# Kernel tuning notes

Hardware: AMD Instinct MI355X
Metric: run time of the kernel (lower is better)

## Reference

```python
import jax, jax.numpy as jnp
import numpy as np

D_MODEL = 512
NHEAD = 8
HEAD_DIM = D_MODEL // NHEAD
DFF = 2048
RANK = 64
L = 1024
N = 8
EPS = 1e-5


def _layer_norm(x, g, b):
    m = jnp.mean(x, axis=-1, keepdims=True)
    v = jnp.mean(jnp.square(x - m), axis=-1, keepdims=True)
    return (x - m) * jax.lax.rsqrt(v + EPS) * g + b


def setup_inputs() -> dict:
    key = jax.random.key(0)
    ks = jax.random.split(key, 20)
    s = 1.0 / np.sqrt(D_MODEL)
    inp = {
        "q": jax.random.normal(ks[0], (L, N, D_MODEL), jnp.float32),
        "k": jax.random.normal(ks[1], (L, N, D_MODEL), jnp.float32),
        "v": jax.random.normal(ks[2], (L, N, D_MODEL), jnp.float32),
        # attention projections, stored (in, out) so x @ W
        "Wq": jax.random.normal(ks[3], (D_MODEL, D_MODEL), jnp.float32) * s,
        "bq": jnp.zeros((D_MODEL,), jnp.float32),
        "Wk": jax.random.normal(ks[4], (D_MODEL, D_MODEL), jnp.float32) * s,
        "bk": jnp.zeros((D_MODEL,), jnp.float32),
        "Wv": jax.random.normal(ks[5], (D_MODEL, D_MODEL), jnp.float32) * s,
        "bv": jnp.zeros((D_MODEL,), jnp.float32),
        "Wo": jax.random.normal(ks[6], (D_MODEL, D_MODEL), jnp.float32) * s,
        "bo": jnp.zeros((D_MODEL,), jnp.float32),
        "topk": jnp.float32(0.3),  # learned scalar, k = int(S * sigmoid(topk))
        "A1": jax.random.normal(ks[7], (D_MODEL, RANK), jnp.float32) * s,
        "B1": jax.random.normal(ks[8], (RANK, DFF), jnp.float32) / np.sqrt(RANK),
        "A2": jax.random.normal(ks[9], (DFF, RANK), jnp.float32) / np.sqrt(DFF),
        "B2": jax.random.normal(ks[10], (RANK, D_MODEL), jnp.float32) / np.sqrt(RANK),
        "g1": jnp.ones((D_MODEL,), jnp.float32),
        "be1": jnp.zeros((D_MODEL,), jnp.float32),
        "g2": jnp.ones((D_MODEL,), jnp.float32),
        "be2": jnp.zeros((D_MODEL,), jnp.float32),
    }
    return inp


def reference(q, k, v, Wq, bq, Wk, bk, Wv, bv, Wo, bo, topk,
              A1, B1, A2, B2, g1, be1, g2, be2):
    Lq, Nb, E = q.shape
    S = k.shape[0]
    H, Dh = NHEAD, HEAD_DIM

    # projections -> (N, L, H, Dh)
    qh = (q @ Wq + bq).reshape(Lq, Nb, H, Dh).transpose(1, 0, 2, 3)
    kh = (k @ Wk + bk).reshape(S, Nb, H, Dh).transpose(1, 0, 2, 3)
    vh = (v @ Wv + bv).reshape(S, Nb, H, Dh).transpose(1, 0, 2, 3)

    scores = jnp.einsum('nlhd,nshd->nlhs', qh, kh) / jnp.sqrt(jnp.float32(Dh))

    # dynamic top-k mask: keep the k = int(S * sigmoid(topk)) largest per row
    k_keep = (S * jax.nn.sigmoid(topk)).astype(jnp.int32)  # 588 for topk=0.3
    sorted_desc = jnp.sort(scores, axis=-1)[..., ::-1]
    idx = jnp.broadcast_to(k_keep - 1, scores.shape[:-1])[..., None]
    thresh = jnp.take_along_axis(sorted_desc, idx, axis=-1)  # k-th largest
    masked = jnp.where(scores >= thresh, scores, -jnp.inf)
    attn_w = jax.nn.softmax(masked, axis=-1)

    # note original flattens (d, h) order: 'nlhs,nshd->nldh' then view(L,N,E)
    ao = jnp.einsum('nlhs,nshd->nldh', attn_w, vh)
    ao = ao.transpose(1, 0, 2, 3).reshape(Lq, Nb, E)
    attn_out = ao @ Wo + bo

    src = _layer_norm(q + attn_out, g1, be1)
    ffn = jax.nn.relu(src @ A1 @ B1) @ A2 @ B2
    src = _layer_norm(src + ffn, g2, be2)
    return src
```

## Files before the change

kernel.cpp:

```cpp
#include <hip/hip_runtime.h>

typedef unsigned short u16;
typedef unsigned int u32;
using s16x8 = __attribute__((ext_vector_type(8))) short;
using s16x4 = __attribute__((ext_vector_type(4))) short;
using u16x4 = __attribute__((ext_vector_type(4))) unsigned short;
using u32x4 = __attribute__((ext_vector_type(4))) unsigned int;
using f32x4 = __attribute__((ext_vector_type(4))) float;

__device__ __forceinline__ u16 f2bf(float f) {
  unsigned int u = __float_as_uint(f);
  u += 0x7FFFu + ((u >> 16) & 1u);
  return (u16)(u >> 16);
}
__device__ __forceinline__ float bf2f(u16 b) {
  return __uint_as_float(((u32)b) << 16);
}
__device__ __forceinline__ u32 pkbf(float a, float b) {
  u32 r;
  asm("v_cvt_pk_bf16_f32 %0, %1, %2" : "=v"(r) : "v"(a), "v"(b));
  return r;
}
__device__ __forceinline__ u32 f2key(float f) {
  u32 u = __float_as_uint(f);
  u32 flip = (u32)((int)u >> 31) | 0x80000000u;
  return (u ^ flip) >> 16;
}
__device__ __forceinline__ float key2f(u32 k) {
  u32 t = k << 16;
  u32 msk = ((int)t < 0) ? 0x80000000u : 0xFFFF0000u;
  return __uint_as_float(t ^ msk);
}

__global__ __launch_bounds__(256) void prep_all(
    const float* __restrict__ q, const float* __restrict__ k, const float* __restrict__ v,
    const float* __restrict__ Wq, const float* __restrict__ Wk, const float* __restrict__ Wv,
    const float* __restrict__ Wo, const float* __restrict__ A1, const float* __restrict__ B1,
    const float* __restrict__ A2, const float* __restrict__ B2,
    u16* __restrict__ qb, u16* __restrict__ kb, u16* __restrict__ vb,
    u16* __restrict__ WqT, u16* __restrict__ WkT, u16* __restrict__ WvT, u16* __restrict__ WoT,
    u16* __restrict__ A1T, u16* __restrict__ B1T, u16* __restrict__ A2T, u16* __restrict__ B2T) {
  __shared__ u16 t[64][68];
  int b = blockIdx.x, tid = threadIdx.x;
  if (b < 12288) {
    const float* src = b < 4096 ? q : (b < 8192 ? k : v);
    u16* dst = b < 4096 ? qb : (b < 8192 ? kb : vb);
    int i = (b & 4095) * 256 + tid;
    float4 f = ((const float4*)src)[i];
    u16x4 o;
    o[0] = f2bf(f.x); o[1] = f2bf(f.y); o[2] = f2bf(f.z); o[3] = f2bf(f.w);
    ((u16x4*)dst)[i] = o;
    return;
  }
  b -= 12288;
  const float* src; u16* dst; int base, R, C;
  if (b < 64)        { src = Wq; dst = WqT; base = 0;   R = 512;  C = 512; }
  else if (b < 128)  { src = Wk; dst = WkT; base = 64;  R = 512;  C = 512; }
  else if (b < 192)  { src = Wv; dst = WvT; base = 128; R = 512;  C = 512; }
  else if (b < 256)  { src = Wo; dst = WoT; base = 192; R = 512;  C = 512; }
  else if (b < 264)  { src = A1; dst = A1T; base = 256; R = 512;  C = 64;  }
  else if (b < 296)  { src = B1; dst = B1T; base = 264; R = 64;   C = 2048;}
  else if (b < 328)  { src = A2; dst = A2T; base = 296; R = 2048; C = 64;  }
  else               { src = B2; dst = B2T; base = 328; R = 64;   C = 512; }
  int ti = b - base;
  int tpr = C >> 6;
  int r0 = (ti / tpr) * 64, c0 = (ti % tpr) * 64;
#pragma unroll
  for (int i = 0; i < 4; ++i) {
    int r = i * 16 + (tid >> 4), c = (tid & 15) * 4;
    float4 f = *(const float4*)&src[(size_t)(r0 + r) * C + c0 + c];
    t[r][c] = f2bf(f.x); t[r][c + 1] = f2bf(f.y);
    t[r][c + 2] = f2bf(f.z); t[r][c + 3] = f2bf(f.w);
  }
  __syncthreads();
#pragma unroll
  for (int i = 0; i < 4; ++i) {
    int cc = i * 16 + (tid >> 4), rr = (tid & 15) * 4;
    u16x4 o;
    o[0] = t[rr][cc]; o[1] = t[rr + 1][cc]; o[2] = t[rr + 2][cc]; o[3] = t[rr + 3][cc];
    *(u16x4*)&dst[(size_t)(c0 + cc) * R + r0 + rr] = o;
  }
}

__global__ __launch_bounds__(256, 4) void qkv_fused(
    const u16* __restrict__ qb, const u16* __restrict__ kb, const u16* __restrict__ vb,
    const u16* __restrict__ WqT, const u16* __restrict__ WkT, const u16* __restrict__ WvT,
    const float* __restrict__ bq, const float* __restrict__ bk, const float* __restrict__ bv,
    u16* __restrict__ Qw, u16* __restrict__ Kw, u16* __restrict__ Vw) {
  __shared__ __align__(16) u16 As[128][72];
  __shared__ __align__(16) u16 Bs[128][72];
  const int z = blockIdx.z;
  const u16* A = z == 0 ? qb : (z == 1 ? kb : vb);
  const u16* Bt = z == 0 ? WqT : (z == 1 ? WkT : WvT);
  const float* bias = z == 0 ? bq : (z == 1 ? bk : bv);
  u16* outp = z == 0 ? Qw : (z == 1 ? Kw : Vw);

  const int tid = threadIdx.x;
  const int m0 = blockIdx.y * 128, n0 = blockIdx.x * 128;
  const int lane = tid & 63, wid = tid >> 6;
  const int l16 = lane & 15, hi = lane >> 4;
  const int wr = (wid >> 1) * 64, wc = (wid & 1) * 64;

  f32x4 acc[4][4];
#pragma unroll
  for (int i = 0; i < 4; ++i)
#pragma unroll
    for (int j = 0; j < 4; ++j) acc[i][j] = (f32x4){0.f, 0.f, 0.f, 0.f};

  for (int k0 = 0; k0 < 512; k0 += 64) {
    if (k0) __syncthreads();
#pragma unroll
    for (int i = 0; i < 4; ++i) {
      int idx = i * 256 + tid;
      int r = idx >> 3, cc = (idx & 7) * 8;
      *(s16x8*)&As[r][cc] = *(const s16x8*)&A[(size_t)(m0 + r) * 512 + k0 + cc];
      *(s16x8*)&Bs[r][cc] = *(const s16x8*)&Bt[(size_t)(n0 + r) * 512 + k0 + cc];
    }
    __syncthreads();
#pragma unroll
    for (int kk = 0; kk < 2; ++kk) {
      const int kb_ = kk * 32 + hi * 8;
      s16x8 af[4], bf[4];
#pragma unroll
      for (int mf = 0; mf < 4; ++mf) af[mf] = *(const s16x8*)&As[wr + mf * 16 + l16][kb_];
#pragma unroll
      for (int nf = 0; nf < 4; ++nf) bf[nf] = *(const s16x8*)&Bs[wc + nf * 16 + l16][kb_];
#pragma unroll
      for (int mf = 0; mf < 4; ++mf)
#pragma unroll
        for (int nf = 0; nf < 4; ++nf)
          acc[mf][nf] = __builtin_amdgcn_mfma_f32_16x16x32_bf16(af[mf], bf[nf], acc[mf][nf], 0, 0, 0);
    }
  }

#pragma unroll
  for (int mf = 0; mf < 4; ++mf)
#pragma unroll
    for (int nf = 0; nf < 4; ++nf)
#pragma unroll
      for (int i = 0; i < 4; ++i) {
        int row = m0 + wr + mf * 16 + hi * 4 + i;
        int col = n0 + wc + nf * 16 + l16;
        float val = acc[mf][nf][i] + bias[col];
        if (z == 0) val *= 0.18033688f;
        int l = row >> 3, n = row & 7, hh = col >> 6, d = col & 63;
        if (z < 2)
          outp[(((size_t)(n * 8 + hh) * 1024 + l) << 6) + d] = f2bf(val);
        else
          outp[((size_t)(n * 8 + hh) * 64 + d) * 1024 + l] = f2bf(val);
      }
}

__global__ __launch_bounds__(512, 4) void attn_kernel(const u16* __restrict__ Qw,
                                                      const u16* __restrict__ Kw,
                                                      const u16* __restrict__ Vw,
                                                      const float* __restrict__ topk,
                                                      u16* __restrict__ ao) {
  __shared__ __align__(16) u16 scb[32 * 1024];
  __shared__ __align__(16) u16 Qt[32][72];
  __shared__ float invs[32];
  const int tid = threadIdx.x, lane = tid & 63, wid = tid >> 6;
  const int l16 = lane & 15, hi = lane >> 4;
  const int mb = blockIdx.x, nh = blockIdx.y;

  const int kkeep = (int)(1024.f / (1.f + __expf(-topk[0])));

  {
    int r = tid >> 4, dc = (tid & 15) << 2;
    *(s16x4*)&Qt[r][dc] =
        *(const s16x4*)&Qw[((size_t)nh * 1024 + mb * 32 + r) * 64 + dc];
  }
  __syncthreads();

  {
    const u16* Kb = Kw + (size_t)nh * 1024 * 64;
    s16x8 bq0[2], bq1[2];
#pragma unroll
    for (int qh = 0; qh < 2; ++qh) {
      bq0[qh] = *(const s16x8*)&Qt[qh * 16 + l16][hi * 8];
      bq1[qh] = *(const s16x8*)&Qt[qh * 16 + l16][32 + hi * 8];
    }
    const int s0 = wid * 128;
    const size_t kbase = (size_t)(s0 + l16) * 64 + hi * 8;
    s16x8 c0 = *(const s16x8*)&Kb[kbase];
    s16x8 c1 = *(const s16x8*)&Kb[kbase + 32];
#pragma unroll
    for (int nf = 0; nf < 8; ++nf) {
      s16x8 n0_, n1_;
      if (nf < 7) {
        const size_t nb = kbase + (size_t)(nf + 1) * 1024;
        n0_ = *(const s16x8*)&Kb[nb];
        n1_ = *(const s16x8*)&Kb[nb + 32];
      }
#pragma unroll
      for (int qh = 0; qh < 2; ++qh) {
        f32x4 acc = {0.f, 0.f, 0.f, 0.f};
        acc = __builtin_amdgcn_mfma_f32_16x16x32_bf16(c0, bq0[qh], acc, 0, 0, 0);
        acc = __builtin_amdgcn_mfma_f32_16x16x32_bf16(c1, bq1[qh], acc, 0, 0, 0);
        const int row_q = qh * 16 + l16;
        u32 k0 = f2key(acc[0]) | (f2key(acc[1]) << 16);
        u32 k1 = f2key(acc[2]) | (f2key(acc[3]) << 16);
        char* rowq = (char*)scb + row_q * 2048;
        int boff = (2 * (s0 + nf * 16 + 4 * hi)) ^ ((row_q & 7) << 4);
        *(uint2*)(rowq + boff) = make_uint2(k0, k1);
      }
      c0 = n0_; c1 = n1_;
    }
  }
  __syncthreads();

  {
    const int r = wid * 4;
    char* rb0 = (char*)scb + (r + 0) * 2048;
    char* rb1 = (char*)scb + (r + 1) * 2048;
    char* rb2 = (char*)scb + (r + 2) * 2048;
    char* rb3 = (char*)scb + (r + 3) * 2048;
    const int X0 = ((r + 0) & 7) << 4, X1 = ((r + 1) & 7) << 4;
    const int X2 = ((r + 2) & 7) << 4, X3 = ((r + 3) & 7) << 4;
    const int o0 = (16 * lane) ^ X0, o0b = (16 * lane + 1024) ^ X0;
    const int o1 = (16 * lane) ^ X1, o1b = (16 * lane + 1024) ^ X1;
    const int o2 = (16 * lane) ^ X2, o2b = (16 * lane + 1024) ^ X2;
    const int o3 = (16 * lane) ^ X3, o3b = (16 * lane + 1024) ^ X3;
    u32x4 q0a = *(const u32x4*)(rb0 + o0), q0b = *(const u32x4*)(rb0 + o0b);
    u32x4 q1a = *(const u32x4*)(rb1 + o1), q1b = *(const u32x4*)(rb1 + o1b);
    u32x4 q2a = *(const u32x4*)(rb2 + o2), q2b = *(const u32x4*)(rb2 + o2b);
    u32x4 q3a = *(const u32x4*)(rb3 + o3), q3b = *(const u32x4*)(rb3 + o3b);
    u32 k0a[16], k1a[16], k2a[16], k3a[16];
#pragma unroll
    for (int j = 0; j < 4; ++j) {
      k0a[2 * j] = q0a[j] & 0xFFFFu; k0a[2 * j + 1] = q0a[j] >> 16;
      k0a[8 + 2 * j] = q0b[j] & 0xFFFFu; k0a[9 + 2 * j] = q0b[j] >> 16;
      k1a[2 * j] = q1a[j] & 0xFFFFu; k1a[2 * j + 1] = q1a[j] >> 16;
      k1a[8 + 2 * j] = q1b[j] & 0xFFFFu; k1a[9 + 2 * j] = q1b[j] >> 16;
      k2a[2 * j] = q2a[j] & 0xFFFFu; k2a[2 * j + 1] = q2a[j] >> 16;
      k2a[8 + 2 * j] = q2b[j] & 0xFFFFu; k2a[9 + 2 * j] = q2b[j] >> 16;
      k3a[2 * j] = q3a[j] & 0xFFFFu; k3a[2 * j + 1] = q3a[j] >> 16;
      k3a[8 + 2 * j] = q3b[j] & 0xFFFFu; k3a[9 + 2 * j] = q3b[j] >> 16;
    }
    u32 T0 = 0, T1 = 0, T2 = 0, T3 = 0;
    for (int bit = 15; bit >= 0; --bit) {
      const u32 bb = 1u << bit;
      u32 c0 = T0 + bb, c1 = T1 + bb, c2 = T2 + bb, c3 = T3 + bb;
      int n0 = 0, n1 = 0, n2 = 0, n3 = 0;
#pragma unroll
      for (int j = 0; j < 16; ++j) {
        n0 += __popcll(__ballot(k0a[j] >= c0));
        n1 += __popcll(__ballot(k1a[j] >= c1));
        n2 += __popcll(__ballot(k2a[j] >= c2));
        n3 += __popcll(__ballot(k3a[j] >= c3));
      }
      T0 = (n0 >= kkeep) ? c0 : T0;
      T1 = (n1 >= kkeep) ? c1 : T1;
      T2 = (n2 >= kkeep) ? c2 : T2;
      T3 = (n3 >= kkeep) ? c3 : T3;
    }
    const float tv0 = key2f(T0), tv1 = key2f(T1), tv2 = key2f(T2), tv3 = key2f(T3);
    float s0 = 0.f, s1 = 0.f, s2 = 0.f, s3 = 0.f;
    u32x4 w0a, w0b, w1a, w1b, w2a_, w2b, w3a, w3b;
#pragma unroll
    for (int j = 0; j < 4; ++j) {
      {
        float e0 = (k0a[2 * j] >= T0) ? __builtin_amdgcn_exp2f(key2f(k0a[2 * j]) - tv0) : 0.f;
        float e1 = (k0a[2 * j + 1] >= T0) ? __builtin_amdgcn_exp2f(key2f(k0a[2 * j + 1]) - tv0) : 0.f;
        float e2 = (k0a[8 + 2 * j] >= T0) ? __builtin_amdgcn_exp2f(key2f(k0a[8 + 2 * j]) - tv0) : 0.f;
        float e3 = (k0a[9 + 2 * j] >= T0) ? __builtin_amdgcn_exp2f(key2f(k0a[9 + 2 * j]) - tv0) : 0.f;
        s0 += e0 + e1 + e2 + e3;
        w0a[j] = pkbf(e0, e1); w0b[j] = pkbf(e2, e3);
      }
      {
        float e0 = (k1a[2 * j] >= T1) ? __builtin_amdgcn_exp2f(key2f(k1a[2 * j]) - tv1) : 0.f;
        float e1 = (k1a[2 * j + 1] >= T1) ? __builtin_amdgcn_exp2f(key2f(k1a[2 * j + 1]) - tv1) : 0.f;
        float e2 = (k1a[8 + 2 * j] >= T1) ? __builtin_amdgcn_exp2f(key2f(k1a[8 + 2 * j]) - tv1) : 0.f;
        float e3 = (k1a[9 + 2 * j] >= T1) ? __builtin_amdgcn_exp2f(key2f(k1a[9 + 2 * j]) - tv1) : 0.f;
        s1 += e0 + e1 + e2 + e3;
        w1a[j] = pkbf(e0, e1); w1b[j] = pkbf(e2, e3);
      }
      {
        float e0 = (k2a[2 * j] >= T2) ? __builtin_amdgcn_exp2f(key2f(k2a[2 * j]) - tv2) : 0.f;
        float e1 = (k2a[2 * j + 1] >= T2) ? __builtin_amdgcn_exp2f(key2f(k2a[2 * j + 1]) - tv2) : 0.f;
        float e2 = (k2a[8 + 2 * j] >= T2) ? __builtin_amdgcn_exp2f(key2f(k2a[8 + 2 * j]) - tv2) : 0.f;
        float e3 = (k2a[9 + 2 * j] >= T2) ? __builtin_amdgcn_exp2f(key2f(k2a[9 + 2 * j]) - tv2) : 0.f;
        s2 += e0 + e1 + e2 + e3;
        w2a_[j] = pkbf(e0, e1); w2b[j] = pkbf(e2, e3);
      }
      {
        float e0 = (k3a[2 * j] >= T3) ? __builtin_amdgcn_exp2f(key2f(k3a[2 * j]) - tv3) : 0.f;
        float e1 = (k3a[2 * j + 1] >= T3) ? __builtin_amdgcn_exp2f(key2f(k3a[2 * j + 1]) - tv3) : 0.f;
        float e2 = (k3a[8 + 2 * j] >= T3) ? __builtin_amdgcn_exp2f(key2f(k3a[8 + 2 * j]) - tv3) : 0.f;
        float e3 = (k3a[9 + 2 * j] >= T3) ? __builtin_amdgcn_exp2f(key2f(k3a[9 + 2 * j]) - tv3) : 0.f;
        s3 += e0 + e1 + e2 + e3;
        w3a[j] = pkbf(e0, e1); w3b[j] = pkbf(e2, e3);
      }
    }
    *(u32x4*)(rb0 + o0) = w0a; *(u32x4*)(rb0 + o0b) = w0b;
    *(u32x4*)(rb1 + o1) = w1a; *(u32x4*)(rb1 + o1b) = w1b;
    *(u32x4*)(rb2 + o2) = w2a_; *(u32x4*)(rb2 + o2b) = w2b;
    *(u32x4*)(rb3 + o3) = w3a; *(u32x4*)(rb3 + o3b) = w3b;
#pragma unroll
    for (int off = 1; off < 64; off <<= 1) {
      s0 += __shfl_xor(s0, off);
      s1 += __shfl_xor(s1, off);
      s2 += __shfl_xor(s2, off);
      s3 += __shfl_xor(s3, off);
    }
    if (lane == 0) {
      invs[r + 0] = __builtin_amdgcn_rcpf(s0);
      invs[r + 1] = __builtin_amdgcn_rcpf(s1);
      invs[r + 2] = __builtin_amdgcn_rcpf(s2);
      invs[r + 3] = __builtin_amdgcn_rcpf(s3);
    }
  }
  __syncthreads();

  {
    const u16* Vb = Vw + (size_t)nh * 64 * 1024;
    const int rh = wid >> 2, d0 = (wid & 3) * 16;
    f32x4 oacc0 = {0.f, 0.f, 0.f, 0.f};
    f32x4 oacc1 = {0.f, 0.f, 0.f, 0.f};
    const char* Pbase = (const char*)scb + (rh * 16 + l16) * 2048;
    const int Xp = (l16 & 7) << 4;
    const size_t vbase = (size_t)(d0 + l16) * 1024 + hi * 8;
    s16x8 v0 = *(const s16x8*)&Vb[vbase];
    s16x8 v1 = *(const s16x8*)&Vb[vbase + 32];
#pragma unroll
    for (int ks = 0; ks < 32; ks += 2) {
      s16x8 nv0, nv1;
      if (ks < 30) {
        nv0 = *(const s16x8*)&Vb[vbase + (size_t)(ks + 2) * 32];
        nv1 = *(const s16x8*)&Vb[vbase + (size_t)(ks + 3) * 32];
      }
      s16x8 a0 = *(const s16x8*)(Pbase + ((ks * 64 + hi * 16) ^ Xp));
      s16x8 a1 = *(const s16x8*)(Pbase + (((ks + 1) * 64 + hi * 16) ^ Xp));
      oacc0 = __builtin_amdgcn_mfma_f32_16x16x32_bf16(a0, v0, oacc0, 0, 0, 0);
      oacc1 = __builtin_amdgcn_mfma_f32_16x16x32_bf16(a1, v1, oacc1, 0, 0, 0);
      v0 = nv0; v1 = nv1;
    }
    const int n = nh >> 3, hh = nh & 7;
#pragma unroll
    for (int i = 0; i < 4; ++i) {
      int l = mb * 32 + rh * 16 + hi * 4 + i;
      int d = d0 + l16;
      float vv = (oacc0[i] + oacc1[i]) * invs[rh * 16 + hi * 4 + i];
      ao[(size_t)(l * 8 + n) * 512 + d * 8 + hh] = f2bf(vv);
    }
  }
}

template <bool FIRST>
__global__ __launch_bounds__(256, 2) void gemm_ln(const u16* __restrict__ A,
                                                  const u16* __restrict__ Bt,
                                                  const float* __restrict__ bias,
                                                  const float* __restrict__ residf,
                                                  const u16* __restrict__ residb,
                                                  const float* __restrict__ g,
                                                  const float* __restrict__ be,
                                                  float* __restrict__ outf,
                                                  u16* __restrict__ outb) {
  constexpr int K = FIRST ? 512 : 64;
  __shared__ __align__(16) u16 As[16][72];
  __shared__ float red_s[4][16];
  __shared__ float red_q[4][16];
  const int tid = threadIdx.x;
  const int lane = tid & 63, wid = tid >> 6;
  const int l16 = lane & 15, hi = lane >> 4;
  const int m0 = blockIdx.x * 16;
  const int wc = wid * 128;

  f32x4 acc[8];
#pragma unroll
  for (int nf = 0; nf < 8; ++nf) acc[nf] = (f32x4){0.f, 0.f, 0.f, 0.f};

  for (int k0 = 0; k0 < K; k0 += 64) {
    if (k0) __syncthreads();
    {
      int r = tid >> 4, c = (tid & 15) << 2;
      *(s16x4*)&As[r][c] = *(const s16x4*)&A[(size_t)(m0 + r) * K + k0 + c];
    }
    __syncthreads();
#pragma unroll
    for (int kk = 0; kk < 2; ++kk) {
      const int kb_ = kk * 32 + hi * 8;
      s16x8 a = *(const s16x8*)&As[l16][kb_];
#pragma unroll
      for (int nf = 0; nf < 8; ++nf) {
        s16x8 b = *(const s16x8*)&Bt[(size_t)(wc + nf * 16 + l16) * K + k0 + kb_];
        acc[nf] = __builtin_amdgcn_mfma_f32_16x16x32_bf16(a, b, acc[nf], 0, 0, 0);
      }
    }
  }

#pragma unroll
  for (int nf = 0; nf < 8; ++nf) {
    int col = wc + nf * 16 + l16;
#pragma unroll
    for (int i = 0; i < 4; ++i) {
      float v = acc[nf][i];
      int row = m0 + hi * 4 + i;
      if (FIRST) v += bias[col] + residf[(size_t)row * 512 + col];
      else v += bf2f(residb[(size_t)row * 512 + col]);
      acc[nf][i] = v;
    }
  }
  float s[4] = {0.f, 0.f, 0.f, 0.f}, q2[4] = {0.f, 0.f, 0.f, 0.f};
#pragma unroll
  for (int nf = 0; nf < 8; ++nf)
#pragma unroll
    for (int i = 0; i < 4; ++i) {
      s[i] += acc[nf][i];
      q2[i] += acc[nf][i] * acc[nf][i];
    }
#pragma unroll
  for (int i = 0; i < 4; ++i) {
#pragma unroll
    for (int off = 1; off < 16; off <<= 1) {
      s[i] += __shfl_xor(s[i], off);
      q2[i] += __shfl_xor(q2[i], off);
    }
  }
  if (l16 == 0) {
#pragma unroll
    for (int i = 0; i < 4; ++i) {
      red_s[wid][hi * 4 + i] = s[i];
      red_q[wid][hi * 4 + i] = q2[i];
    }
  }
  __syncthreads();
  float mean[4], rstd[4];
#pragma unroll
  for (int i = 0; i < 4; ++i) {
    int r = hi * 4 + i;
    float ms = red_s[0][r] + red_s[1][r] + red_s[2][r] + red_s[3][r];
    float mq = red_q[0][r] + red_q[1][r] + red_q[2][r] + red_q[3][r];
    mean[i] = ms * (1.f / 512.f);
    float var = mq * (1.f / 512.f) - mean[i] * mean[i];
    rstd[i] = rsqrtf(var + 1e-5f);
  }
#pragma unroll
  for (int nf = 0; nf < 8; ++nf) {
    int col = wc + nf * 16 + l16;
    float gv = g[col], bev = be[col];
#pragma unroll
    for (int i = 0; i < 4; ++i) {
      int row = m0 + hi * 4 + i;
      float y = (acc[nf][i] - mean[i]) * rstd[i] * gv + bev;
      if (FIRST) outb[(size_t)row * 512 + col] = f2bf(y);
      else outf[(size_t)row * 512 + col] = y;
    }
  }
}

__global__ __launch_bounds__(256, 4) void ffn3(const u16* __restrict__ srcb,
                                               const u16* __restrict__ A1T,
                                               const u16* __restrict__ B1T,
                                               const u16* __restrict__ A2T,
                                               u16* __restrict__ w2) {
  __shared__ __align__(16) u16 As[32][72];
  __shared__ __align__(16) u16 Bs[64][72];
  __shared__ __align__(16) u16 Us[32][72];
  __shared__ __align__(16) u16 B1s[64][72];
  __shared__ __align__(16) u16 A2s[64][72];
  __shared__ __align__(16) u16 Hs[32][72];
  const int tid = threadIdx.x;
  const int lane = tid & 63, wid = tid >> 6;
  const int l16 = lane & 15, hi = lane >> 4;
  const int m0 = blockIdx.x * 32;
  const int wm = (wid & 1) * 16, wn = (wid >> 1) * 32;

  f32x4 accu[2];
  accu[0] = (f32x4){0.f, 0.f, 0.f, 0.f};
  accu[1] = (f32x4){0.f, 0.f, 0.f, 0.f};
  for (int k0 = 0; k0 < 512; k0 += 64) {
    if (k0) __syncthreads();
    {
      int r = tid >> 3, c = (tid & 7) << 3;
      *(s16x8*)&As[r][c] = *(const s16x8*)&srcb[(size_t)(m0 + r) * 512 + k0 + c];
    }
#pragma unroll
    for (int i = 0; i < 2; ++i) {
      int idx = i * 256 + tid;
      int r = idx >> 3, c = (idx & 7) << 3;
      *(s16x8*)&Bs[r][c] = *(const s16x8*)&A1T[(size_t)r * 512 + k0 + c];
    }
    __syncthreads();
#pragma unroll
    for (int kk = 0; kk < 2; ++kk) {
      const int kb_ = kk * 32 + hi * 8;
      s16x8 a = *(const s16x8*)&As[wm + l16][kb_];
#pragma unroll
      for (int j = 0; j < 2; ++j) {
        s16x8 b = *(const s16x8*)&Bs[wn + j * 16 + l16][kb_];
        accu[j] = __builtin_amdgcn_mfma_f32_16x16x32_bf16(a, b, accu[j], 0, 0, 0);
      }
    }
  }
  __syncthreads();
#pragma unroll
  for (int j = 0; j < 2; ++j)
#pragma unroll
    for (int i = 0; i < 4; ++i)
      Us[wm + hi * 4 + i][wn + j * 16 + l16] = f2bf(accu[j][i]);

  f32x4 w2a[2];
  w2a[0] = (f32x4){0.f, 0.f, 0.f, 0.f};
  w2a[1] = (f32x4){0.f, 0.f, 0.f, 0.f};
  for (int jc = 0; jc < 32; ++jc) {
#pragma unroll
    for (int i = 0; i < 2; ++i) {
      int idx = i * 256 + tid;
      int r = idx >> 3, c = (idx & 7) << 3;
      *(s16x8*)&B1s[r][c] = *(const s16x8*)&B1T[(size_t)(jc * 64 + r) * 64 + c];
      *(s16x8*)&A2s[r][c] = *(const s16x8*)&A2T[(size_t)r * 2048 + jc * 64 + c];
    }
    __syncthreads();
    f32x4 ha[2];
    ha[0] = (f32x4){0.f, 0.f, 0.f, 0.f};
    ha[1] = (f32x4){0.f, 0.f, 0.f, 0.f};
#pragma unroll
    for (int kk = 0; kk < 2; ++kk) {
      const int kb_ = kk * 32 + hi * 8;
      s16x8 a = *(const s16x8*)&Us[wm + l16][kb_];
#pragma unroll
      for (int j = 0; j < 2; ++j) {
        s16x8 b = *(const s16x8*)&B1s[wn + j * 16 + l16][kb_];
        ha[j] = __builtin_amdgcn_mfma_f32_16x16x32_bf16(a, b, ha[j], 0, 0, 0);
      }
    }
#pragma unroll
    for (int j = 0; j < 2; ++j)
#pragma unroll
      for (int i = 0; i < 4; ++i)
        Hs[wm + hi * 4 + i][wn + j * 16 + l16] = f2bf(fmaxf(ha[j][i], 0.f));
    __syncthreads();
#pragma unroll
    for (int kk = 0; kk < 2; ++kk) {
      const int kb_ = kk * 32 + hi * 8;
      s16x8 a = *(const s16x8*)&Hs[wm + l16][kb_];
#pragma unroll
      for (int j = 0; j < 2; ++j) {
        s16x8 b = *(const s16x8*)&A2s[wn + j * 16 + l16][kb_];
        w2a[j] = __builtin_amdgcn_mfma_f32_16x16x32_bf16(a, b, w2a[j], 0, 0, 0);
      }
    }
    __syncthreads();
  }
#pragma unroll
  for (int j = 0; j < 2; ++j)
#pragma unroll
    for (int i = 0; i < 4; ++i)
      w2[(size_t)(m0 + wm + hi * 4 + i) * 64 + wn + j * 16 + l16] = f2bf(w2a[j][i]);
}

extern "C" void kernel_launch(void* const* d_in, const int* in_sizes, int n_in,
                              void* d_out, int out_size, void* d_ws, size_t ws_size,
                              hipStream_t stream) {
  const float* q = (const float*)d_in[0];
  const float* k = (const float*)d_in[1];
  const float* v = (const float*)d_in[2];
  const float* Wq = (const float*)d_in[3];
  const float* bq = (const float*)d_in[4];
  const float* Wk = (const float*)d_in[5];
  const float* bk = (const float*)d_in[6];
  const float* Wv = (const float*)d_in[7];
  const float* bv = (const float*)d_in[8];
  const float* Wo = (const float*)d_in[9];
  const float* bo = (const float*)d_in[10];
  const float* topk = (const float*)d_in[11];
  const float* A1 = (const float*)d_in[12];
  const float* B1 = (const float*)d_in[13];
  const float* A2 = (const float*)d_in[14];
  const float* B2 = (const float*)d_in[15];
  const float* g1 = (const float*)d_in[16];
  const float* be1 = (const float*)d_in[17];
  const float* g2 = (const float*)d_in[18];
  const float* be2 = (const float*)d_in[19];

  char* ws = (char*)d_ws;
  constexpr size_t SZ_TOK_BF = (size_t)8192 * 512 * 2;
  constexpr size_t SZ_W_BF = (size_t)512 * 512 * 2;
  constexpr size_t O_QB = 0;
  constexpr size_t O_KB = O_QB + SZ_TOK_BF;
  constexpr size_t O_VB = O_KB + SZ_TOK_BF;
  constexpr size_t O_QW = O_VB + SZ_TOK_BF;
  constexpr size_t O_KW = O_QW + SZ_TOK_BF;
  constexpr size_t O_VW = O_KW + SZ_TOK_BF;
  constexpr size_t O_WQT = O_VW + SZ_TOK_BF;
  constexpr size_t O_WKT = O_WQT + SZ_W_BF;
  constexpr size_t O_WVT = O_WKT + SZ_W_BF;
  constexpr size_t O_WOT = O_WVT + SZ_W_BF;
  constexpr size_t O_A1T = O_WOT + SZ_W_BF;
  constexpr size_t O_B1T = O_A1T + 65536;
  constexpr size_t O_A2T = O_B1T + 262144;
  constexpr size_t O_B2T = O_A2T + 262144;
  constexpr size_t O_AO = O_B2T + 65536;
  constexpr size_t O_SRCB = O_AO + SZ_TOK_BF;
  constexpr size_t O_W2 = O_SRCB + SZ_TOK_BF;

  u16* qb = (u16*)(ws + O_QB);
  u16* kb = (u16*)(ws + O_KB);
  u16* vb = (u16*)(ws + O_VB);
  u16* Qw_ = (u16*)(ws + O_QW);
  u16* Kw_ = (u16*)(ws + O_KW);
  u16* Vw_ = (u16*)(ws + O_VW);
  u16* WqT = (u16*)(ws + O_WQT);
  u16* WkT = (u16*)(ws + O_WKT);
  u16* WvT = (u16*)(ws + O_WVT);
  u16* WoT = (u16*)(ws + O_WOT);
  u16* A1T = (u16*)(ws + O_A1T);
  u16* B1T = (u16*)(ws + O_B1T);
  u16* A2T = (u16*)(ws + O_A2T);
  u16* B2T = (u16*)(ws + O_B2T);
  u16* ao = (u16*)(ws + O_AO);
  u16* srcb = (u16*)(ws + O_SRCB);
  u16* w2 = (u16*)(ws + O_W2);

  prep_all<<<12624, 256, 0, stream>>>(q, k, v, Wq, Wk, Wv, Wo, A1, B1, A2, B2,
                                      qb, kb, vb, WqT, WkT, WvT, WoT, A1T, B1T, A2T, B2T);

  qkv_fused<<<dim3(4, 64, 3), 256, 0, stream>>>(qb, kb, vb, WqT, WkT, WvT,
                                                bq, bk, bv, Qw_, Kw_, Vw_);

  attn_kernel<<<dim3(32, 64), 512, 0, stream>>>(Qw_, Kw_, Vw_, topk, ao);

  gemm_ln<true><<<512, 256, 0, stream>>>(ao, WoT, bo, q, nullptr, g1, be1, nullptr, srcb);

  ffn3<<<256, 256, 0, stream>>>(srcb, A1T, B1T, A2T, w2);

  gemm_ln<false><<<512, 256, 0, stream>>>(w2, B2T, nullptr, nullptr, srcb, g2, be2,
                                          (float*)d_out, nullptr);
}
```

Before: 291.3 us.

## Halve attention query tile to 16 rows and use scalar-mask compare for top-k count

The attention kernel now processes 16 query rows per block instead of 32, halving LDS use and per-wave register state (2 rows per wave in the top-k radix search instead of 4). The launch bound is raised to allow more resident blocks, and the grid doubles. The ballot+popcount is replaced with an inline v_cmp writing an SGPR mask directly. In exchange, K and V tiles are reloaded twice as often per head, and only half the waves do the PV matmul.

```diff
diff --git a/kernel.cpp b/kernel.cpp
--- a/kernel.cpp
+++ b/kernel.cpp
@@ -2,6 +2,7 @@
 
 typedef unsigned short u16;
 typedef unsigned int u32;
+typedef unsigned long long u64;
 using s16x8 = __attribute__((ext_vector_type(8))) short;
 using s16x4 = __attribute__((ext_vector_type(4))) short;
 using u16x4 = __attribute__((ext_vector_type(4))) unsigned short;
@@ -20,6 +21,11 @@
   u32 r;
   asm("v_cvt_pk_bf16_f32 %0, %1, %2" : "=v"(r) : "v"(a), "v"(b));
   return r;
+}
+__device__ __forceinline__ u64 cmp_ge(u32 key, u32 cand) {
+  u64 m;
+  asm("v_cmp_le_u32 %0, %1, %2" : "=s"(m) : "s"(cand), "v"(key));
+  return m;
 }
 __device__ __forceinline__ u32 f2key(float f) {
   u32 u = __float_as_uint(f);
@@ -151,39 +157,37 @@
       }
 }
 
-__global__ __launch_bounds__(512, 4) void attn_kernel(const u16* __restrict__ Qw,
+__global__ __launch_bounds__(512, 8) void attn_kernel(const u16* __restrict__ Qw,
                                                       const u16* __restrict__ Kw,
                                                       const u16* __restrict__ Vw,
                                                       const float* __restrict__ topk,
                                                       u16* __restrict__ ao) {
-  __shared__ __align__(16) u16 scb[32 * 1024];
-  __shared__ __align__(16) u16 Qt[32][72];
-  __shared__ float invs[32];
+  __shared__ __align__(16) u16 scb[16 * 1024];
+  __shared__ __align__(16) u16 Qt[16][72];
+  __shared__ float invs[16];
   const int tid = threadIdx.x, lane = tid & 63, wid = tid >> 6;
   const int l16 = lane & 15, hi = lane >> 4;
   const int mb = blockIdx.x, nh = blockIdx.y;
 
   const int kkeep = (int)(1024.f / (1.f + __expf(-topk[0])));
 
-  {
+  if (tid < 256) {
     int r = tid >> 4, dc = (tid & 15) << 2;
     *(s16x4*)&Qt[r][dc] =
-        *(const s16x4*)&Qw[((size_t)nh * 1024 + mb * 32 + r) * 64 + dc];
+        *(const s16x4*)&Qw[((size_t)nh * 1024 + mb * 16 + r) * 64 + dc];
   }
   __syncthreads();
 
   {
     const u16* Kb = Kw + (size_t)nh * 1024 * 64;
-    s16x8 bq0[2], bq1[2];
-#pragma unroll
-    for (int qh = 0; qh < 2; ++qh) {
-      bq0[qh] = *(const s16x8*)&Qt[qh * 16 + l16][hi * 8];
-      bq1[qh] = *(const s16x8*)&Qt[qh * 16 + l16][32 + hi * 8];
-    }
+    s16x8 bq0 = *(const s16x8*)&Qt[l16][hi * 8];
+    s16x8 bq1 = *(const s16x8*)&Qt[l16][32 + hi * 8];
     const int s0 = wid * 128;
     const size_t kbase = (size_t)(s0 + l16) * 64 + hi * 8;
     s16x8 c0 = *(const s16x8*)&Kb[kbase];
     s16x8 c1 = *(const s16x8*)&Kb[kbase + 32];
+    char* rowq = (char*)scb + l16 * 2048;
+    const int Xq = (l16 & 7) << 4;
 #pragma unroll
     for (int nf = 0; nf < 8; ++nf) {
       s16x8 n0_, n1_;
@@ -192,71 +196,51 @@
         n0_ = *(const s16x8*)&Kb[nb];
         n1_ = *(const s16x8*)&Kb[nb + 32];
       }
-#pragma unroll
-      for (int qh = 0; qh < 2; ++qh) {
-        f32x4 acc = {0.f, 0.f, 0.f, 0.f};
-        acc = __builtin_amdgcn_mfma_f32_16x16x32_bf16(c0, bq0[qh], acc, 0, 0, 0);
-        acc = __builtin_amdgcn_mfma_f32_16x16x32_bf16(c1, bq1[qh], acc, 0, 0, 0);
-        const int row_q = qh * 16 + l16;
-        u32 k0 = f2key(acc[0]) | (f2key(acc[1]) << 16);
-        u32 k1 = f2key(acc[2]) | (f2key(acc[3]) << 16);
-        char* rowq = (char*)scb + row_q * 2048;
-        int boff = (2 * (s0 + nf * 16 + 4 * hi)) ^ ((row_q & 7) << 4);
-        *(uint2*)(rowq + boff) = make_uint2(k0, k1);
-      }
+      f32x4 acc = {0.f, 0.f, 0.f, 0.f};
+      acc = __builtin_amdgcn_mfma_f32_16x16x32_bf16(c0, bq0, acc, 0, 0, 0);
+      acc = __builtin_amdgcn_mfma_f32_16x16x32_bf16(c1, bq1, acc, 0, 0, 0);
+      u32 k0 = f2key(acc[0]) | (f2key(acc[1]) << 16);
+      u32 k1 = f2key(acc[2]) | (f2key(acc[3]) << 16);
+      int boff = (2 * (s0 + nf * 16 + 4 * hi)) ^ Xq;
+      *(uint2*)(rowq + boff) = make_uint2(k0, k1);
       c0 = n0_; c1 = n1_;
     }
   }
   __syncthreads();
 
   {
-    const int r = wid * 4;
-    char* rb0 = (char*)scb + (r + 0) * 2048;
-    char* rb1 = (char*)scb + (r + 1) * 2048;
-    char* rb2 = (char*)scb + (r + 2) * 2048;
-    char* rb3 = (char*)scb + (r + 3) * 2048;
-    const int X0 = ((r + 0) & 7) << 4, X1 = ((r + 1) & 7) << 4;
-    const int X2 = ((r + 2) & 7) << 4, X3 = ((r + 3) & 7) << 4;
+    const int r0 = wid * 2, r1 = r0 + 1;
+    char* rb0 = (char*)scb + r0 * 2048;
+    char* rb1 = (char*)scb + r1 * 2048;
+    const int X0 = (r0 & 7) << 4, X1 = (r1 & 7) << 4;
     const int o0 = (16 * lane) ^ X0, o0b = (16 * lane + 1024) ^ X0;
     const int o1 = (16 * lane) ^ X1, o1b = (16 * lane + 1024) ^ X1;
-    const int o2 = (16 * lane) ^ X2, o2b = (16 * lane + 1024) ^ X2;
-    const int o3 = (16 * lane) ^ X3, o3b = (16 * lane + 1024) ^ X3;
     u32x4 q0a = *(const u32x4*)(rb0 + o0), q0b = *(const u32x4*)(rb0 + o0b);
     u32x4 q1a = *(const u32x4*)(rb1 + o1), q1b = *(const u32x4*)(rb1 + o1b);
-    u32x4 q2a = *(const u32x4*)(rb2 + o2), q2b = *(const u32x4*)(rb2 + o2b);
-    u32x4 q3a = *(const u32x4*)(rb3 + o3), q3b = *(const u32x4*)(rb3 + o3b);
-    u32 k0a[16], k1a[16], k2a[16], k3a[16];
+    u32 k0a[16], k1a[16];
 #pragma unroll
     for (int j = 0; j < 4; ++j) {
       k0a[2 * j] = q0a[j] & 0xFFFFu; k0a[2 * j + 1] = q0a[j] >> 16;
       k0a[8 + 2 * j] = q0b[j] & 0xFFFFu; k0a[9 + 2 * j] = q0b[j] >> 16;
       k1a[2 * j] = q1a[j] & 0xFFFFu; k1a[2 * j + 1] = q1a[j] >> 16;
       k1a[8 + 2 * j] = q1b[j] & 0xFFFFu; k1a[9 + 2 * j] = q1b[j] >> 16;
-      k2a[2 * j] = q2a[j] & 0xFFFFu; k2a[2 * j + 1] = q2a[j] >> 16;
-      k2a[8 + 2 * j] = q2b[j] & 0xFFFFu; k2a[9 + 2 * j] = q2b[j] >> 16;
-      k3a[2 * j] = q3a[j] & 0xFFFFu; k3a[2 * j + 1] = q3a[j] >> 16;
-      k3a[8 + 2 * j] = q3b[j] & 0xFFFFu; k3a[9 + 2 * j] = q3b[j] >> 16;
-    }
-    u32 T0 = 0, T1 = 0, T2 = 0, T3 = 0;
+    }
+    u32 T0 = 0, T1 = 0;
     for (int bit = 15; bit >= 0; --bit) {
       const u32 bb = 1u << bit;
-      u32 c0 = T0 + bb, c1 = T1 + bb, c2 = T2 + bb, c3 = T3 + bb;
-      int n0 = 0, n1 = 0, n2 = 0, n3 = 0;
+      u32 c0 = T0 + bb, c1 = T1 + bb;
+      int n0 = 0, n1 = 0;
 #pragma unroll
       for (int j = 0; j < 16; ++j) {
-        n0 += __popcll(__ballot(k0a[j] >= c0));
-        n1 += __popcll(__ballot(k1a[j] >= c1));
-        n2 += __popcll(__ballot(k2a[j] >= c2));
-        n3 += __popcll(__ballot(k3a[j] >= c3));
+        n0 += __builtin_popcountll(cmp_ge(k0a[j], c0));
+        n1 += __builtin_popcountll(cmp_ge(k1a[j], c1));
       }
       T0 = (n0 >= kkeep) ? c0 : T0;
       T1 = (n1 >= kkeep) ? c1 : T1;
-      T2 = (n2 >= kkeep) ? c2 : T2;
-      T3 = (n3 >= kkeep) ? c3 : T3;
-    }
-    const float tv0 = key2f(T0), tv1 = key2f(T1), tv2 = key2f(T2), tv3 = key2f(T3);
-    float s0 = 0.f, s1 = 0.f, s2 = 0.f, s3 = 0.f;
-    u32x4 w0a, w0b, w1a, w1b, w2a_, w2b, w3a, w3b;
+    }
+    const float tv0 = key2f(T0), tv1 = key2f(T1);
+    float s0 = 0.f, s1 = 0.f;
+    u32x4 w0a, w0b, w1a, w1b;
 #pragma unroll
     for (int j = 0; j < 4; ++j) {
       {
@@ -275,49 +259,27 @@
         s1 += e0 + e1 + e2 + e3;
         w1a[j] = pkbf(e0, e1); w1b[j] = pkbf(e2, e3);
       }
-      {
-        float e0 = (k2a[2 * j] >= T2) ? __builtin_amdgcn_exp2f(key2f(k2a[2 * j]) - tv2) : 0.f;
-        float e1 = (k2a[2 * j + 1] >= T2) ? __builtin_amdgcn_exp2f(key2f(k2a[2 * j + 1]) - tv2) : 0.f;
-        float e2 = (k2a[8 + 2 * j] >= T2) ? __builtin_amdgcn_exp2f(key2f(k2a[8 + 2 * j]) - tv2) : 0.f;
-        float e3 = (k2a[9 + 2 * j] >= T2) ? __builtin_amdgcn_exp2f(key2f(k2a[9 + 2 * j]) - tv2) : 0.f;
-        s2 += e0 + e1 + e2 + e3;
-        w2a_[j] = pkbf(e0, e1); w2b[j] = pkbf(e2, e3);
-      }
-      {
-        float e0 = (k3a[2 * j] >= T3) ? __builtin_amdgcn_exp2f(key2f(k3a[2 * j]) - tv3) : 0.f;
-        float e1 = (k3a[2 * j + 1] >= T3) ? __builtin_amdgcn_exp2f(key2f(k3a[2 * j + 1]) - tv3) : 0.f;
-        float e2 = (k3a[8 + 2 * j] >= T3) ? __builtin_amdgcn_exp2f(key2f(k3a[8 + 2 * j]) - tv3) : 0.f;
-        float e3 = (k3a[9 + 2 * j] >= T3) ? __builtin_amdgcn_exp2f(key2f(k3a[9 + 2 * j]) - tv3) : 0.f;
-        s3 += e0 + e1 + e2 + e3;
-        w3a[j] = pkbf(e0, e1); w3b[j] = pkbf(e2, e3);
-      }
     }
     *(u32x4*)(rb0 + o0) = w0a; *(u32x4*)(rb0 + o0b) = w0b;
     *(u32x4*)(rb1 + o1) = w1a; *(u32x4*)(rb1 + o1b) = w1b;
-    *(u32x4*)(rb2 + o2) = w2a_; *(u32x4*)(rb2 + o2b) = w2b;
-    *(u32x4*)(rb3 + o3) = w3a; *(u32x4*)(rb3 + o3b) = w3b;
 #pragma unroll
     for (int off = 1; off < 64; off <<= 1) {
       s0 += __shfl_xor(s0, off);
       s1 += __shfl_xor(s1, off);
-      s2 += __shfl_xor(s2, off);
-      s3 += __shfl_xor(s3, off);
     }
     if (lane == 0) {
-      invs[r + 0] = __builtin_amdgcn_rcpf(s0);
-      invs[r + 1] = __builtin_amdgcn_rcpf(s1);
-      invs[r + 2] = __builtin_amdgcn_rcpf(s2);
-      invs[r + 3] = __builtin_amdgcn_rcpf(s3);
+      invs[r0] = __builtin_amdgcn_rcpf(s0);
+      invs[r1] = __builtin_amdgcn_rcpf(s1);
     }
   }
   __syncthreads();
 
-  {
+  if (wid < 4) {
     const u16* Vb = Vw + (size_t)nh * 64 * 1024;
-    const int rh = wid >> 2, d0 = (wid & 3) * 16;
+    const int d0 = wid * 16;
     f32x4 oacc0 = {0.f, 0.f, 0.f, 0.f};
     f32x4 oacc1 = {0.f, 0.f, 0.f, 0.f};
-    const char* Pbase = (const char*)scb + (rh * 16 + l16) * 2048;
+    const char* Pbase = (const char*)scb + l16 * 2048;
     const int Xp = (l16 & 7) << 4;
     const size_t vbase = (size_t)(d0 + l16) * 1024 + hi * 8;
     s16x8 v0 = *(const s16x8*)&Vb[vbase];
@@ -338,9 +300,9 @@
     const int n = nh >> 3, hh = nh & 7;
 #pragma unroll
     for (int i = 0; i < 4; ++i) {
-      int l = mb * 32 + rh * 16 + hi * 4 + i;
+      int l = mb * 16 + hi * 4 + i;
       int d = d0 + l16;
-      float vv = (oacc0[i] + oacc1[i]) * invs[rh * 16 + hi * 4 + i];
+      float vv = (oacc0[i] + oacc1[i]) * invs[hi * 4 + i];
       ao[(size_t)(l * 8 + n) * 512 + d * 8 + hh] = f2bf(vv);
     }
   }
@@ -619,7 +581,7 @@
   qkv_fused<<<dim3(4, 64, 3), 256, 0, stream>>>(qb, kb, vb, WqT, WkT, WvT,
                                                 bq, bk, bv, Qw_, Kw_, Vw_);
 
-  attn_kernel<<<dim3(32, 64), 512, 0, stream>>>(Qw_, Kw_, Vw_, topk, ao);
+  attn_kernel<<<dim3(64, 64), 512, 0, stream>>>(Qw_, Kw_, Vw_, topk, ao);
 
   gemm_ln<true><<<512, 256, 0, stream>>>(ao, WoT, bo, q, nullptr, g1, be1, nullptr, srcb);
 
```

Result: no change. 287.0 us (-1.5%).
